# Kernel optimization log

Measured on AMD Instinct MI355X. Metric: run time of the kernel, lower is better.

Reference implementation:

```python
import jax, jax.numpy as jnp
import numpy as np

NUM_M = 512
NUM_T = 64
MAX_STEPS = 20
TAU = 1.0


def setup_inputs() -> dict:
    key = jax.random.key(0)
    ks = jax.random.split(key, 10)
    num_m, num_t = NUM_M, NUM_T
    inp = {
        "v_src": jax.random.normal(ks[0], (1, num_m), jnp.float32),
        "v_target": jax.random.normal(ks[1], (1, num_m), jnp.float32),
        # small-magnitude generators so matrix_exp stays well-conditioned
        "omegas": jax.random.normal(ks[2], (num_t, num_m, num_m), jnp.float32) * 0.01,
        "W1": jax.random.normal(ks[3], (2 * num_m, 256), jnp.float32) * (1.0 / np.sqrt(2 * num_m)),
        "b1": jnp.zeros((256,), jnp.float32),
        "W2": jax.random.normal(ks[4], (256, 128), jnp.float32) * (1.0 / np.sqrt(256)),
        "b2": jnp.zeros((128,), jnp.float32),
        "W3": jax.random.normal(ks[5], (128, num_t), jnp.float32) * (1.0 / np.sqrt(128)),
        "b3": jnp.zeros((num_t,), jnp.float32),
        # pre-sampled gumbel noise, one draw per step: [max_steps, B, num_t]
        "gumbel_noise": jax.random.gumbel(ks[6], (MAX_STEPS, 1, num_t), jnp.float32),
    }
    return inp


def reference(v_src, v_target, omegas, W1, b1, W2, b2, W3, b3, gumbel_noise):
    tgt_idx = jnp.argmax(v_target, axis=-1)  # [B]

    def mlp(x):
        h = jax.nn.relu(x @ W1 + b1)
        h = jax.nn.relu(h @ W2 + b2)
        return h @ W3 + b3  # [B, num_t]

    batched_expm = jax.vmap(jax.scipy.linalg.expm)

    def step(carry, g):
        v, done = carry  # v: [B, num_m], done: [B] bool
        x = jnp.concatenate([v, v_target], axis=-1)        # [B, 2*num_m]
        logits = mlp(x)                                     # [B, num_t]
        # gumbel_softmax(tau=1.0, hard=False)
        soft = jax.nn.softmax((logits + g) / TAU, axis=-1)
        omega_k = jnp.einsum('bt,tmk->bmk', soft, omegas)   # [B, m, m]
        R_k = batched_expm(omega_k)                         # [B, m, m]
        v_new = jnp.einsum('bmk,bk->bm', R_k, v)            # [B, m]
        # freeze state and zero-pad logits once the target marking was reached
        v_out = jnp.where(done[:, None], v, v_new)
        logits_out = jnp.where(done[:, None], jnp.zeros_like(logits), logits)
        done_new = done | (jnp.argmax(v_new, axis=-1) == tgt_idx)
        return (v_out, done_new), logits_out

    done0 = jnp.zeros((v_src.shape[0],), bool)
    (v_final, _), logits_seq = jax.lax.scan(step, (v_src, done0), gumbel_noise)
    # logits_seq: [max_steps, B, num_t]; B==1 -> [max_steps, num_t] (torch squeeze(0))
    return v_final, logits_seq[:, 0, :]
```

## Files before the change

kernel.cpp:

```cpp
#include <hip/hip_runtime.h>
#include <hip/hip_fp16.h>


#define NBLK 256
#define NTHR 512
#define NSTEP 20
#define NTAY 3
#define RBUF 4

typedef unsigned long long ull;

#define XW(buf, i) (X + ((((buf) << 8) + (i)) << 3))

__device__ __forceinline__ float wredsum(float p) {
#pragma unroll
  for (int off = 32; off > 0; off >>= 1) p += __shfl_xor(p, off, 64);
  return p;
}

__device__ __forceinline__ void wredsum2(float& p0, float& p1) {
#pragma unroll
  for (int off = 32; off > 0; off >>= 1) {
    float t0 = __shfl_xor(p0, off, 64);
    float t1 = __shfl_xor(p1, off, 64);
    p0 += t0;
    p1 += t1;
  }
}

__device__ __forceinline__ void publish2(ull* w, float v0, float v1, unsigned int tag2) {
  unsigned int u0 = (__float_as_uint(v0) & ~3u) | tag2;
  ull x = (ull)u0 | ((ull)__float_as_uint(v1) << 32);
  __hip_atomic_store(w, x, __ATOMIC_RELAXED, __HIP_MEMORY_SCOPE_AGENT);
}

__device__ __forceinline__ float2 poll2(ull* w, unsigned int tag2) {
  int it = 0;
  for (;;) {
    ull x = __hip_atomic_load(w, __ATOMIC_RELAXED, __HIP_MEMORY_SCOPE_AGENT);
    if ((unsigned int)(x & 3u) == tag2) {
      float2 r;
      r.x = __uint_as_float((unsigned int)x);
      r.y = __uint_as_float((unsigned int)(x >> 32));
      return r;
    }
    if (it == 0)      __builtin_amdgcn_s_sleep(1);
    else if (it == 1) __builtin_amdgcn_s_sleep(2);
    else              __builtin_amdgcn_s_sleep(4);
    if (it < 2) ++it;
  }
}

__device__ __forceinline__ void poll8(ull* w0, unsigned int tg, float* o) {
  ull x0 = 0, x1 = 0, x2 = 0, x3 = 0;
  bool g0 = false, g1 = false, g2 = false, g3 = false;
  int it = 0;
  for (;;) {
    if (!g0) { ull x = __hip_atomic_load(w0,      __ATOMIC_RELAXED, __HIP_MEMORY_SCOPE_AGENT); if ((unsigned int)(x & 3u) == tg) { x0 = x; g0 = true; } }
    if (!g1) { ull x = __hip_atomic_load(w0 + 8,  __ATOMIC_RELAXED, __HIP_MEMORY_SCOPE_AGENT); if ((unsigned int)(x & 3u) == tg) { x1 = x; g1 = true; } }
    if (!g2) { ull x = __hip_atomic_load(w0 + 16, __ATOMIC_RELAXED, __HIP_MEMORY_SCOPE_AGENT); if ((unsigned int)(x & 3u) == tg) { x2 = x; g2 = true; } }
    if (!g3) { ull x = __hip_atomic_load(w0 + 24, __ATOMIC_RELAXED, __HIP_MEMORY_SCOPE_AGENT); if ((unsigned int)(x & 3u) == tg) { x3 = x; g3 = true; } }
    if (g0 && g1 && g2 && g3) break;
    if (it == 0)      __builtin_amdgcn_s_sleep(1);
    else if (it == 1) __builtin_amdgcn_s_sleep(2);
    else              __builtin_amdgcn_s_sleep(4);
    if (it < 2) ++it;
  }
  o[0] = __uint_as_float((unsigned int)x0); o[1] = __uint_as_float((unsigned int)(x0 >> 32));
  o[2] = __uint_as_float((unsigned int)x1); o[3] = __uint_as_float((unsigned int)(x1 >> 32));
  o[4] = __uint_as_float((unsigned int)x2); o[5] = __uint_as_float((unsigned int)(x2 >> 32));
  o[6] = __uint_as_float((unsigned int)x3); o[7] = __uint_as_float((unsigned int)(x3 >> 32));
}

__global__ __launch_bounds__(NTHR) void petri_kernel(
    const float* __restrict__ vsrc, const float* __restrict__ vtgt,
    const float* __restrict__ omg,  const float* __restrict__ W1,
    const float* __restrict__ b1,   const float* __restrict__ W2,
    const float* __restrict__ b2,   const float* __restrict__ W3,
    const float* __restrict__ b3,   const float* __restrict__ gum,
    ull* __restrict__ X, float* __restrict__ out) {
  __shared__ __half2 oh[64 * 512];
  __shared__ __align__(16) float A0_s[512];
  __shared__ __align__(16) float A1_s[512];
  __shared__ __align__(16) float v_loc[512];
  __shared__ float tgt_s[512];
  __shared__ float w1c_s[1024];
  __shared__ float gum_s[NSTEP * 64];
  __shared__ float b2_s[128], b3_s[64];
  __shared__ float soft_s[64], h1_s[256], h2_s[128];
  __shared__ float redp[512];
  __shared__ float rf8[8];
  __shared__ int   ri8[8];
  __shared__ float cB_s[1];
  __shared__ int   bc[1];

  const int b = blockIdx.x, tid = threadIdx.x;
  const int wv = tid >> 6, ln = tid & 63;

  v_loc[tid] = vsrc[tid];
  tgt_s[tid] = vtgt[tid];
  w1c_s[tid] = W1[tid * 256 + b];
  w1c_s[tid + 512] = W1[(tid + 512) * 256 + b];
  for (int i = tid; i < NSTEP * 64; i += NTHR) gum_s[i] = gum[i];
  if (tid >= NTHR - 128) {
    int j = tid - (NTHR - 128);
    b2_s[j] = b2[j];
    if (j < 64) b3_s[j] = b3[j];
  }
  float w2r[64];
  {
    const int o = tid & 127, q = tid >> 7;
    const float* p = W2 + ((q << 6) * 128) + o;
#pragma unroll
    for (int i = 0; i < 64; ++i) w2r[i] = p[i * 128];
  }
  float w3r[16];
  {
    const int o = tid & 63, q = tid >> 6;
    const float* p = W3 + ((q << 4) * 64) + o;
#pragma unroll
    for (int i = 0; i < 16; ++i) w3r[i] = p[i * 64];
  }
  {
    const int tq = tid >> 7;
    const int c4 = (tid & 127) << 2;
    const float* rp = omg + (b << 10) + c4;
#pragma unroll 4
    for (int g = 0; g < 16; ++g) {
      const int t = (g << 2) + tq;
      const float* p = rp + t * 262144;
      const float4 f0 = *(const float4*)(p);
      const float4 f1 = *(const float4*)(p + 512);
      __half2* dst = oh + t * 512 + c4;
      dst[0] = __floats2half2_rn(f0.x, f1.x);
      dst[1] = __floats2half2_rn(f0.y, f1.y);
      dst[2] = __floats2half2_rn(f0.z, f1.z);
      dst[3] = __floats2half2_rn(f0.w, f1.w);
    }
  }
  __syncthreads();

  {
    float p = tgt_s[tid] * w1c_s[tid + 512];
    p = wredsum(p);
    if (ln == 0) rf8[wv] = p;
    __syncthreads();
    if (tid == 0) {
      float a = b1[b];
      for (int q = 0; q < 8; ++q) a += rf8[q];
      cB_s[0] = a;
    }
    __syncthreads();
  }

  int tgtIdx;
  {
    float v = tgt_s[tid]; int ix = tid;
#pragma unroll
    for (int off = 32; off > 0; off >>= 1) {
      float ov = __shfl_xor(v, off, 64); int oi = __shfl_xor(ix, off, 64);
      if (ov > v || (ov == v && oi < ix)) { v = ov; ix = oi; }
    }
    if (ln == 0) { rf8[wv] = v; ri8[wv] = ix; }
    __syncthreads();
    if (tid == 0) {
      float bv = rf8[0]; int bix = ri8[0];
      for (int q = 1; q < 8; ++q)
        if (rf8[q] > bv || (rf8[q] == bv && ri8[q] < bix)) { bv = rf8[q]; bix = ri8[q]; }
      bc[0] = bix;
    }
    __syncthreads();
    tgtIdx = bc[0];
    __syncthreads();
  }

  float vreg[8], w1t[8];
  if (wv == 0) {
    const int l8 = ln << 3;
#pragma unroll
    for (int k = 0; k < 8; ++k) { vreg[k] = v_loc[l8 + k]; w1t[k] = w1c_s[l8 + k]; }
  }

  int d = 0;
  int r = 0;

  for (int s = 0; s < NSTEP; ++s) {
    if (d) {
      if (b == 0 && tid < 64) out[512 + s * 64 + tid] = 0.0f;
      continue;
    }

    {
      const int buf = r & (RBUF - 1);
      const unsigned int tg = (unsigned int)((r >> 2) & 3);
      if (wv == 0) {
        float p = 0.f;
#pragma unroll
        for (int k = 0; k < 8; ++k) p = fmaf(vreg[k], w1t[k], p);
        p = wredsum(p);
        if (ln == 0) {
          float h = fmaxf(p + cB_s[0], 0.f);
          publish2(XW(buf, b), h, h, tg);
        }
      }
      if (tid < 256) h1_s[tid] = poll2(XW(buf, tid), tg).x;
      __syncthreads();
      ++r;
    }

    {
      const int q = tid >> 7;
      float a = 0.f;
      const float* hp = h1_s + (q << 6);
#pragma unroll
      for (int i = 0; i < 64; ++i) a = fmaf(hp[i], w2r[i], a);
      redp[tid] = a;
    }
    __syncthreads();
    if (tid < 128) {
      float rr = redp[tid] + redp[tid + 128] + redp[tid + 256] + redp[tid + 384] + b2_s[tid];
      h2_s[tid] = fmaxf(rr, 0.f);
    }
    __syncthreads();
    {
      const int q = tid >> 6;
      float a = 0.f;
      const float* hp = h2_s + (q << 4);
#pragma unroll
      for (int i = 0; i < 16; ++i) a = fmaf(hp[i], w3r[i], a);
      redp[tid] = a;
    }
    __syncthreads();
    if (tid < 64) {
      float a = b3_s[tid];
#pragma unroll
      for (int q = 0; q < 8; ++q) a += redp[tid + (q << 6)];
      float lg = a + gum_s[s * 64 + tid];
      float mx = lg;
#pragma unroll
      for (int off = 32; off > 0; off >>= 1) mx = fmaxf(mx, __shfl_xor(mx, off, 64));
      float e = __expf(lg - mx);
      float sm = e;
#pragma unroll
      for (int off = 32; off > 0; off >>= 1) sm += __shfl_xor(sm, off, 64);
      soft_s[tid] = e / sm;
      if (b == 0) out[512 + s * 64 + tid] = a;
    }
    __syncthreads();

    {
      float a0 = 0.f, a1 = 0.f;
#pragma unroll 8
      for (int t = 0; t < 64; ++t) {
        float2 xy = __half22float2(oh[t * 512 + tid]);
        float sv = soft_s[t];
        a0 = fmaf(sv, xy.x, a0);
        a1 = fmaf(sv, xy.y, a1);
      }
      A0_s[tid] = a0; A1_s[tid] = a1;
    }
    __syncthreads();

    if (wv == 0) {
      const int l8 = ln << 3;
      float wreg[8];
#pragma unroll
      for (int k = 0; k < 8; ++k) wreg[k] = vreg[k];
      float acc0 = 0.f, acc1 = 0.f;
#pragma unroll
      for (int n = 1; n <= NTAY; ++n) {
        const int rr = r + (n - 1);
        const int buf = rr & (RBUF - 1);
        const unsigned int tg = (unsigned int)((rr >> 2) & 3);
        const float4 a00 = *(const float4*)(A0_s + l8);
        const float4 a01 = *(const float4*)(A0_s + l8 + 4);
        const float4 a10 = *(const float4*)(A1_s + l8);
        const float4 a11 = *(const float4*)(A1_s + l8 + 4);
        float p0 = 0.f, p1 = 0.f;
        p0 = fmaf(a00.x, wreg[0], p0); p0 = fmaf(a00.y, wreg[1], p0);
        p0 = fmaf(a00.z, wreg[2], p0); p0 = fmaf(a00.w, wreg[3], p0);
        p0 = fmaf(a01.x, wreg[4], p0); p0 = fmaf(a01.y, wreg[5], p0);
        p0 = fmaf(a01.z, wreg[6], p0); p0 = fmaf(a01.w, wreg[7], p0);
        p1 = fmaf(a10.x, wreg[0], p1); p1 = fmaf(a10.y, wreg[1], p1);
        p1 = fmaf(a10.z, wreg[2], p1); p1 = fmaf(a10.w, wreg[3], p1);
        p1 = fmaf(a11.x, wreg[4], p1); p1 = fmaf(a11.y, wreg[5], p1);
        p1 = fmaf(a11.z, wreg[6], p1); p1 = fmaf(a11.w, wreg[7], p1);
        wredsum2(p0, p1);
        if (ln == 0) {
          float s0, s1;
          if (n == 1) {
            s0 = p0; s1 = p1;
            acc0 = v_loc[(b << 1)] + s0;
            acc1 = v_loc[(b << 1) + 1] + s1;
          } else {
            const float inv = (n == 2) ? 0.5f : (1.0f / 3.0f);
            s0 = p0 * inv; s1 = p1 * inv;
            acc0 += s0; acc1 += s1;
          }
          const float q0 = (n < NTAY) ? s0 : acc0;
          const float q1 = (n < NTAY) ? s1 : acc1;
          publish2(XW(buf, b), q0, q1, tg);
        }
        poll8(XW(buf, (ln << 2)), tg, wreg);
      }
#pragma unroll
      for (int k = 0; k < 8; ++k) vreg[k] = wreg[k];
      *(float4*)(v_loc + l8)     = make_float4(wreg[0], wreg[1], wreg[2], wreg[3]);
      *(float4*)(v_loc + l8 + 4) = make_float4(wreg[4], wreg[5], wreg[6], wreg[7]);
      float mv = wreg[0]; int mi = l8;
#pragma unroll
      for (int k = 1; k < 8; ++k) if (wreg[k] > mv) { mv = wreg[k]; mi = l8 + k; }
#pragma unroll
      for (int off = 32; off > 0; off >>= 1) {
        float ov = __shfl_xor(mv, off, 64); int oi = __shfl_xor(mi, off, 64);
        if (ov > mv || (ov == mv && oi < mi)) { mv = ov; mi = oi; }
      }
      if (ln == 0) bc[0] = (mi == tgtIdx) ? 1 : 0;
    }
    __syncthreads();
    if (bc[0]) d = 1;
    r += NTAY;
  }

  if (b == 0) out[tid] = v_loc[tid];
}

extern "C" void kernel_launch(void* const* d_in, const int* in_sizes, int n_in,
                              void* d_out, int out_size, void* d_ws, size_t ws_size,
                              hipStream_t stream) {
  (void)in_sizes; (void)n_in; (void)out_size; (void)ws_size;
  petri_kernel<<<dim3(NBLK), dim3(NTHR), 0, stream>>>(
      (const float*)d_in[0], (const float*)d_in[1], (const float*)d_in[2],
      (const float*)d_in[3], (const float*)d_in[4], (const float*)d_in[5],
      (const float*)d_in[6], (const float*)d_in[7], (const float*)d_in[8],
      (const float*)d_in[9], (ull*)d_ws, (float*)d_out);
}
```

Baseline: 343.0 us.

## Fuse next-step first MLP layer into expm exchange via fixed-point atomic accumulation

Each block now scatters its two new state entries, multiplied by its rows of W1, into global 64-bit accumulators using fixed-point atomicAdds that pack a count and a biased integer sum. Waves 1-4 poll these accumulators to build the next step's h1 while wave 0 finishes the Taylor exchange, which removes the separate per-step publish/poll round for layer 1. It also splits dot-product accumulators for ILP and swizzles the A0/A1 shared-memory layout so the float4 reads stay hoisted out of the Taylor loop. The fixed-point quantization of h1 changes numerics slightly and adds atomic contention across 256 blocks.

Result: slower. 962.1 us (+180.5%).

```diff
diff --git a/kernel.cpp b/kernel.cpp
--- a/kernel.cpp
+++ b/kernel.cpp
@@ -11,6 +11,11 @@
 typedef unsigned long long ull;
 
 #define XW(buf, i) (X + ((((buf) << 8) + (i)) << 3))
+#define AW(p, i)   (X + 8192 + ((((p) << 8) + (i)) << 3))
+
+#define SCALE_F   4194304.0f
+#define INV_SCALE 2.384185791015625e-07f
+#define M44 ((1ull << 44) - 1)
 
 __device__ __forceinline__ float wredsum(float p) {
 #pragma unroll
@@ -85,13 +90,15 @@
   __shared__ __align__(16) float v_loc[512];
   __shared__ float tgt_s[512];
   __shared__ float w1c_s[1024];
+  __shared__ float w1r0_s[256], w1r1_s[256];
+  __shared__ float cB_s[256];
   __shared__ float gum_s[NSTEP * 64];
   __shared__ float b2_s[128], b3_s[64];
   __shared__ float soft_s[64], h1_s[256], h2_s[128];
   __shared__ float redp[512];
-  __shared__ float rf8[8];
+  __shared__ float rf8[8], rf8b[8];
   __shared__ int   ri8[8];
-  __shared__ float cB_s[1];
+  __shared__ int   goflag;
   __shared__ int   bc[1];
 
   const int b = blockIdx.x, tid = threadIdx.x;
@@ -101,11 +108,18 @@
   tgt_s[tid] = vtgt[tid];
   w1c_s[tid] = W1[tid * 256 + b];
   w1c_s[tid + 512] = W1[(tid + 512) * 256 + b];
+  if (tid < 256) w1r0_s[tid] = W1[(b << 1) * 256 + tid];
+  else           w1r1_s[tid - 256] = W1[((b << 1) + 1) * 256 + (tid - 256)];
   for (int i = tid; i < NSTEP * 64; i += NTHR) gum_s[i] = gum[i];
   if (tid >= NTHR - 128) {
     int j = tid - (NTHR - 128);
     b2_s[j] = b2[j];
     if (j < 64) b3_s[j] = b3[j];
+  }
+  if (tid == 0) {
+    goflag = 0;
+    __hip_atomic_store(AW(0, b), 0ull, __ATOMIC_RELAXED, __HIP_MEMORY_SCOPE_AGENT);
+    __hip_atomic_store(AW(1, b), 0ull, __ATOMIC_RELAXED, __HIP_MEMORY_SCOPE_AGENT);
   }
   float w2r[64];
   {
@@ -141,14 +155,21 @@
   __syncthreads();
 
   {
-    float p = tgt_s[tid] * w1c_s[tid + 512];
-    p = wredsum(p);
-    if (ln == 0) rf8[wv] = p;
+    float p0 = tgt_s[tid] * w1c_s[tid + 512];
+    float p1 = v_loc[tid] * w1c_s[tid];
+    wredsum2(p0, p1);
+    if (ln == 0) { rf8[wv] = p0; rf8b[wv] = p1; }
     __syncthreads();
     if (tid == 0) {
-      float a = b1[b];
-      for (int q = 0; q < 8; ++q) a += rf8[q];
-      cB_s[0] = a;
+      float cB = b1[b], dv = 0.f;
+      for (int q = 0; q < 8; ++q) { cB += rf8[q]; dv += rf8b[q]; }
+      float h0 = fmaxf(dv + cB, 0.f);
+      publish2(XW(0, b), h0, cB, 0u);
+    }
+    if (tid < 256) {
+      float2 g = poll2(XW(0, tid), 0u);
+      h1_s[tid] = g.x;
+      cB_s[tid] = g.y;
     }
     __syncthreads();
   }
@@ -174,15 +195,17 @@
     __syncthreads();
   }
 
-  float vreg[8], w1t[8];
+  float vreg[8];
   if (wv == 0) {
     const int l8 = ln << 3;
 #pragma unroll
-    for (int k = 0; k < 8; ++k) { vreg[k] = v_loc[l8 + k]; w1t[k] = w1c_s[l8 + k]; }
-  }
+    for (int k = 0; k < 8; ++k) vreg[k] = v_loc[l8 + k];
+  }
+
+  ull prevA = 0, prevB = 0, expA = 0, expB = 0;
 
   int d = 0;
-  int r = 0;
+  int r = 1;
 
   for (int s = 0; s < NSTEP; ++s) {
     if (d) {
@@ -191,30 +214,17 @@
     }
 
     {
-      const int buf = r & (RBUF - 1);
-      const unsigned int tg = (unsigned int)((r >> 2) & 3);
-      if (wv == 0) {
-        float p = 0.f;
-#pragma unroll
-        for (int k = 0; k < 8; ++k) p = fmaf(vreg[k], w1t[k], p);
-        p = wredsum(p);
-        if (ln == 0) {
-          float h = fmaxf(p + cB_s[0], 0.f);
-          publish2(XW(buf, b), h, h, tg);
-        }
-      }
-      if (tid < 256) h1_s[tid] = poll2(XW(buf, tid), tg).x;
-      __syncthreads();
-      ++r;
-    }
-
-    {
       const int q = tid >> 7;
-      float a = 0.f;
       const float* hp = h1_s + (q << 6);
-#pragma unroll
-      for (int i = 0; i < 64; ++i) a = fmaf(hp[i], w2r[i], a);
-      redp[tid] = a;
+      float a0 = 0.f, a1 = 0.f, a2 = 0.f, a3 = 0.f;
+#pragma unroll
+      for (int i = 0; i < 64; i += 4) {
+        a0 = fmaf(hp[i],     w2r[i],     a0);
+        a1 = fmaf(hp[i + 1], w2r[i + 1], a1);
+        a2 = fmaf(hp[i + 2], w2r[i + 2], a2);
+        a3 = fmaf(hp[i + 3], w2r[i + 3], a3);
+      }
+      redp[tid] = (a0 + a1) + (a2 + a3);
     }
     __syncthreads();
     if (tid < 128) {
@@ -224,11 +234,14 @@
     __syncthreads();
     {
       const int q = tid >> 6;
-      float a = 0.f;
       const float* hp = h2_s + (q << 4);
-#pragma unroll
-      for (int i = 0; i < 16; ++i) a = fmaf(hp[i], w3r[i], a);
-      redp[tid] = a;
+      float a0 = 0.f, a1 = 0.f;
+#pragma unroll
+      for (int i = 0; i < 16; i += 2) {
+        a0 = fmaf(hp[i],     w3r[i],     a0);
+        a1 = fmaf(hp[i + 1], w3r[i + 1], a1);
+      }
+      redp[tid] = a0 + a1;
     }
     __syncthreads();
     if (tid < 64) {
@@ -249,20 +262,33 @@
     __syncthreads();
 
     {
-      float a0 = 0.f, a1 = 0.f;
+      float a0 = 0.f, a1 = 0.f, c0 = 0.f, c1 = 0.f;
 #pragma unroll 8
-      for (int t = 0; t < 64; ++t) {
-        float2 xy = __half22float2(oh[t * 512 + tid]);
-        float sv = soft_s[t];
-        a0 = fmaf(sv, xy.x, a0);
-        a1 = fmaf(sv, xy.y, a1);
-      }
-      A0_s[tid] = a0; A1_s[tid] = a1;
+      for (int t = 0; t < 64; t += 2) {
+        float2 xy0 = __half22float2(oh[t * 512 + tid]);
+        float2 xy1 = __half22float2(oh[(t + 1) * 512 + tid]);
+        float s0 = soft_s[t], s1 = soft_s[t + 1];
+        a0 = fmaf(s0, xy0.x, a0);
+        c0 = fmaf(s0, xy0.y, c0);
+        a1 = fmaf(s1, xy1.x, a1);
+        c1 = fmaf(s1, xy1.y, c1);
+      }
+      const int kk = tid >> 2;
+      const int sj = ((kk ^ ((kk >> 3) & 7)) << 2) | (tid & 3);
+      A0_s[sj] = a0 + a1;
+      A1_s[sj] = c0 + c1;
     }
     __syncthreads();
 
     if (wv == 0) {
-      const int l8 = ln << 3;
+      const int xh = (ln >> 2) & 7;
+      const int p0i = (ln << 1) ^ xh;
+      const int p1i = ((ln << 1) + 1) ^ xh;
+      const float4* A0p = (const float4*)A0_s;
+      const float4* A1p = (const float4*)A1_s;
+      const float4 a00 = A0p[p0i], a01 = A0p[p1i];
+      const float4 a10 = A1p[p0i], a11 = A1p[p1i];
+      const float vb0 = v_loc[b << 1], vb1 = v_loc[(b << 1) + 1];
       float wreg[8];
 #pragma unroll
       for (int k = 0; k < 8; ++k) wreg[k] = vreg[k];
@@ -272,10 +298,6 @@
         const int rr = r + (n - 1);
         const int buf = rr & (RBUF - 1);
         const unsigned int tg = (unsigned int)((rr >> 2) & 3);
-        const float4 a00 = *(const float4*)(A0_s + l8);
-        const float4 a01 = *(const float4*)(A0_s + l8 + 4);
-        const float4 a10 = *(const float4*)(A1_s + l8);
-        const float4 a11 = *(const float4*)(A1_s + l8 + 4);
         float p0 = 0.f, p1 = 0.f;
         p0 = fmaf(a00.x, wreg[0], p0); p0 = fmaf(a00.y, wreg[1], p0);
         p0 = fmaf(a00.z, wreg[2], p0); p0 = fmaf(a00.w, wreg[3], p0);
@@ -290,8 +312,7 @@
           float s0, s1;
           if (n == 1) {
             s0 = p0; s1 = p1;
-            acc0 = v_loc[(b << 1)] + s0;
-            acc1 = v_loc[(b << 1) + 1] + s1;
+            acc0 = vb0 + s0; acc1 = vb1 + s1;
           } else {
             const float inv = (n == 2) ? 0.5f : (1.0f / 3.0f);
             s0 = p0 * inv; s1 = p1 * inv;
@@ -301,8 +322,23 @@
           const float q1 = (n < NTAY) ? s1 : acc1;
           publish2(XW(buf, b), q0, q1, tg);
         }
+        if (n == NTAY && s < NSTEP - 1) {
+          const float ac0 = __shfl(acc0, 0, 64);
+          const float ac1 = __shfl(acc1, 0, 64);
+          const int p = (s + 1) & 1;
+#pragma unroll
+          for (int k = 0; k < 4; ++k) {
+            const int j = (ln << 2) + k;
+            const float part = fmaf(ac0, w1r0_s[j], ac1 * w1r1_s[j]);
+            const int iv = __float2int_rn(part * SCALE_F) + (1 << 30);
+            atomicAdd(AW(p, j), (1ull << 44) + (ull)(unsigned)iv);
+          }
+        }
         poll8(XW(buf, (ln << 2)), tg, wreg);
-      }
+        if (n == 2 && ln == 0)
+          __hip_atomic_store(&goflag, s + 1, __ATOMIC_RELAXED, __HIP_MEMORY_SCOPE_WORKGROUP);
+      }
+      const int l8 = ln << 3;
 #pragma unroll
       for (int k = 0; k < 8; ++k) vreg[k] = wreg[k];
       *(float4*)(v_loc + l8)     = make_float4(wreg[0], wreg[1], wreg[2], wreg[3]);
@@ -316,6 +352,31 @@
         if (ov > mv || (ov == mv && oi < mi)) { mv = ov; mi = oi; }
       }
       if (ln == 0) bc[0] = (mi == tgtIdx) ? 1 : 0;
+    } else if (wv <= 4) {
+      if (s < NSTEP - 1) {
+        while (__hip_atomic_load(&goflag, __ATOMIC_RELAXED, __HIP_MEMORY_SCOPE_WORKGROUP) != s + 1)
+          __builtin_amdgcn_s_sleep(2);
+        const int j = ((wv - 1) << 6) + ln;
+        const int p = (s + 1) & 1;
+        ull target;
+        if (p) { expB += 256; target = expB; } else { expA += 256; target = expA; }
+        ull* w = AW(p, j);
+        ull x;
+        int it = 0;
+        for (;;) {
+          x = __hip_atomic_load(w, __ATOMIC_RELAXED, __HIP_MEMORY_SCOPE_AGENT);
+          if ((x >> 44) == target) break;
+          if (it == 0)      __builtin_amdgcn_s_sleep(1);
+          else if (it == 1) __builtin_amdgcn_s_sleep(2);
+          else              __builtin_amdgcn_s_sleep(4);
+          if (it < 2) ++it;
+        }
+        const ull pv = p ? prevB : prevA;
+        const long long dl = (long long)((x & M44) - (pv & M44));
+        const float h = (float)(dl - (256ll << 30)) * INV_SCALE + cB_s[j];
+        h1_s[j] = fmaxf(h, 0.f);
+        if (p) prevB = x; else prevA = x;
+      }
     }
     __syncthreads();
     if (bc[0]) d = 1;
```

## Pack exchange slots densely, hoist next-step h1 publish, buffer logits in LDS

Applied to the files above, without the earlier changes.

Exchange slots in the global workspace are packed contiguously instead of spread 64 bytes apart, so the four polled words share cache lines. The first-layer partial for the next step is computed and published right after the Taylor exchange rather than at the start of the next iteration, which removes one serial phase from the critical path. Logits are kept in shared memory and written once at the end, and the inner dot products use split accumulators to shorten FMA dependency chains. Dense packing may add false sharing between blocks writing neighbouring slots.

Result: slower. 381.8 us (+11.3%).

```diff
diff --git a/kernel.cpp b/kernel.cpp
--- a/kernel.cpp
+++ b/kernel.cpp
@@ -10,7 +10,7 @@
 
 typedef unsigned long long ull;
 
-#define XW(buf, i) (X + ((((buf) << 8) + (i)) << 3))
+#define XW(buf, i) (X + ((buf) << 8) + (i))
 
 __device__ __forceinline__ float wredsum(float p) {
 #pragma unroll
@@ -56,10 +56,10 @@
   bool g0 = false, g1 = false, g2 = false, g3 = false;
   int it = 0;
   for (;;) {
-    if (!g0) { ull x = __hip_atomic_load(w0,      __ATOMIC_RELAXED, __HIP_MEMORY_SCOPE_AGENT); if ((unsigned int)(x & 3u) == tg) { x0 = x; g0 = true; } }
-    if (!g1) { ull x = __hip_atomic_load(w0 + 8,  __ATOMIC_RELAXED, __HIP_MEMORY_SCOPE_AGENT); if ((unsigned int)(x & 3u) == tg) { x1 = x; g1 = true; } }
-    if (!g2) { ull x = __hip_atomic_load(w0 + 16, __ATOMIC_RELAXED, __HIP_MEMORY_SCOPE_AGENT); if ((unsigned int)(x & 3u) == tg) { x2 = x; g2 = true; } }
-    if (!g3) { ull x = __hip_atomic_load(w0 + 24, __ATOMIC_RELAXED, __HIP_MEMORY_SCOPE_AGENT); if ((unsigned int)(x & 3u) == tg) { x3 = x; g3 = true; } }
+    if (!g0) { ull x = __hip_atomic_load(w0,     __ATOMIC_RELAXED, __HIP_MEMORY_SCOPE_AGENT); if ((unsigned int)(x & 3u) == tg) { x0 = x; g0 = true; } }
+    if (!g1) { ull x = __hip_atomic_load(w0 + 1, __ATOMIC_RELAXED, __HIP_MEMORY_SCOPE_AGENT); if ((unsigned int)(x & 3u) == tg) { x1 = x; g1 = true; } }
+    if (!g2) { ull x = __hip_atomic_load(w0 + 2, __ATOMIC_RELAXED, __HIP_MEMORY_SCOPE_AGENT); if ((unsigned int)(x & 3u) == tg) { x2 = x; g2 = true; } }
+    if (!g3) { ull x = __hip_atomic_load(w0 + 3, __ATOMIC_RELAXED, __HIP_MEMORY_SCOPE_AGENT); if ((unsigned int)(x & 3u) == tg) { x3 = x; g3 = true; } }
     if (g0 && g1 && g2 && g3) break;
     if (it == 0)      __builtin_amdgcn_s_sleep(1);
     else if (it == 1) __builtin_amdgcn_s_sleep(2);
@@ -89,6 +89,7 @@
   __shared__ float b2_s[128], b3_s[64];
   __shared__ float soft_s[64], h1_s[256], h2_s[128];
   __shared__ float redp[512];
+  __shared__ float llog[NSTEP * 64];
   __shared__ float rf8[8];
   __shared__ int   ri8[8];
   __shared__ float cB_s[1];
@@ -179,30 +180,27 @@
     const int l8 = ln << 3;
 #pragma unroll
     for (int k = 0; k < 8; ++k) { vreg[k] = v_loc[l8 + k]; w1t[k] = w1c_s[l8 + k]; }
+    float p = 0.f;
+#pragma unroll
+    for (int k = 0; k < 8; ++k) p = fmaf(vreg[k], w1t[k], p);
+    p = wredsum(p);
+    if (ln == 0) {
+      float h = fmaxf(p + cB_s[0], 0.f);
+      publish2(XW(0, b), h, h, 0u);
+    }
   }
 
   int d = 0;
+  int nAct = 0;
   int r = 0;
 
   for (int s = 0; s < NSTEP; ++s) {
-    if (d) {
-      if (b == 0 && tid < 64) out[512 + s * 64 + tid] = 0.0f;
-      continue;
-    }
+    if (d) continue;
+    nAct = s + 1;
 
     {
       const int buf = r & (RBUF - 1);
       const unsigned int tg = (unsigned int)((r >> 2) & 3);
-      if (wv == 0) {
-        float p = 0.f;
-#pragma unroll
-        for (int k = 0; k < 8; ++k) p = fmaf(vreg[k], w1t[k], p);
-        p = wredsum(p);
-        if (ln == 0) {
-          float h = fmaxf(p + cB_s[0], 0.f);
-          publish2(XW(buf, b), h, h, tg);
-        }
-      }
       if (tid < 256) h1_s[tid] = poll2(XW(buf, tid), tg).x;
       __syncthreads();
       ++r;
@@ -210,11 +208,16 @@
 
     {
       const int q = tid >> 7;
-      float a = 0.f;
       const float* hp = h1_s + (q << 6);
-#pragma unroll
-      for (int i = 0; i < 64; ++i) a = fmaf(hp[i], w2r[i], a);
-      redp[tid] = a;
+      float a0 = 0.f, a1 = 0.f, a2 = 0.f, a3 = 0.f;
+#pragma unroll
+      for (int i = 0; i < 64; i += 4) {
+        a0 = fmaf(hp[i],     w2r[i],     a0);
+        a1 = fmaf(hp[i + 1], w2r[i + 1], a1);
+        a2 = fmaf(hp[i + 2], w2r[i + 2], a2);
+        a3 = fmaf(hp[i + 3], w2r[i + 3], a3);
+      }
+      redp[tid] = (a0 + a1) + (a2 + a3);
     }
     __syncthreads();
     if (tid < 128) {
@@ -224,11 +227,14 @@
     __syncthreads();
     {
       const int q = tid >> 6;
-      float a = 0.f;
       const float* hp = h2_s + (q << 4);
-#pragma unroll
-      for (int i = 0; i < 16; ++i) a = fmaf(hp[i], w3r[i], a);
-      redp[tid] = a;
+      float a0 = 0.f, a1 = 0.f;
+#pragma unroll
+      for (int i = 0; i < 16; i += 2) {
+        a0 = fmaf(hp[i],     w3r[i],     a0);
+        a1 = fmaf(hp[i + 1], w3r[i + 1], a1);
+      }
+      redp[tid] = a0 + a1;
     }
     __syncthreads();
     if (tid < 64) {
@@ -244,25 +250,34 @@
 #pragma unroll
       for (int off = 32; off > 0; off >>= 1) sm += __shfl_xor(sm, off, 64);
       soft_s[tid] = e / sm;
-      if (b == 0) out[512 + s * 64 + tid] = a;
+      llog[s * 64 + tid] = a;
     }
     __syncthreads();
 
     {
-      float a0 = 0.f, a1 = 0.f;
+      float a0 = 0.f, a1 = 0.f, c0 = 0.f, c1 = 0.f;
 #pragma unroll 8
-      for (int t = 0; t < 64; ++t) {
-        float2 xy = __half22float2(oh[t * 512 + tid]);
-        float sv = soft_s[t];
-        a0 = fmaf(sv, xy.x, a0);
-        a1 = fmaf(sv, xy.y, a1);
-      }
-      A0_s[tid] = a0; A1_s[tid] = a1;
+      for (int t = 0; t < 64; t += 2) {
+        float2 xy0 = __half22float2(oh[t * 512 + tid]);
+        float2 xy1 = __half22float2(oh[(t + 1) * 512 + tid]);
+        float s0 = soft_s[t], s1 = soft_s[t + 1];
+        a0 = fmaf(s0, xy0.x, a0);
+        c0 = fmaf(s0, xy0.y, c0);
+        a1 = fmaf(s1, xy1.x, a1);
+        c1 = fmaf(s1, xy1.y, c1);
+      }
+      A0_s[tid] = a0 + a1;
+      A1_s[tid] = c0 + c1;
     }
     __syncthreads();
 
     if (wv == 0) {
       const int l8 = ln << 3;
+      const float4 a00 = *(const float4*)(A0_s + l8);
+      const float4 a01 = *(const float4*)(A0_s + l8 + 4);
+      const float4 a10 = *(const float4*)(A1_s + l8);
+      const float4 a11 = *(const float4*)(A1_s + l8 + 4);
+      const float vb0 = v_loc[b << 1], vb1 = v_loc[(b << 1) + 1];
       float wreg[8];
 #pragma unroll
       for (int k = 0; k < 8; ++k) wreg[k] = vreg[k];
@@ -272,10 +287,6 @@
         const int rr = r + (n - 1);
         const int buf = rr & (RBUF - 1);
         const unsigned int tg = (unsigned int)((rr >> 2) & 3);
-        const float4 a00 = *(const float4*)(A0_s + l8);
-        const float4 a01 = *(const float4*)(A0_s + l8 + 4);
-        const float4 a10 = *(const float4*)(A1_s + l8);
-        const float4 a11 = *(const float4*)(A1_s + l8 + 4);
         float p0 = 0.f, p1 = 0.f;
         p0 = fmaf(a00.x, wreg[0], p0); p0 = fmaf(a00.y, wreg[1], p0);
         p0 = fmaf(a00.z, wreg[2], p0); p0 = fmaf(a00.w, wreg[3], p0);
@@ -290,8 +301,7 @@
           float s0, s1;
           if (n == 1) {
             s0 = p0; s1 = p1;
-            acc0 = v_loc[(b << 1)] + s0;
-            acc1 = v_loc[(b << 1) + 1] + s1;
+            acc0 = vb0 + s0; acc1 = vb1 + s1;
           } else {
             const float inv = (n == 2) ? 0.5f : (1.0f / 3.0f);
             s0 = p0 * inv; s1 = p1 * inv;
@@ -303,6 +313,18 @@
         }
         poll8(XW(buf, (ln << 2)), tg, wreg);
       }
+      if (s + 1 < NSTEP) {
+        const int rh = r + NTAY;
+        const unsigned int tgh = (unsigned int)((rh >> 2) & 3);
+        float ph = 0.f;
+#pragma unroll
+        for (int k = 0; k < 8; ++k) ph = fmaf(wreg[k], w1t[k], ph);
+        ph = wredsum(ph);
+        if (ln == 0) {
+          float h = fmaxf(ph + cB_s[0], 0.f);
+          publish2(XW(rh & (RBUF - 1), b), h, h, tgh);
+        }
+      }
 #pragma unroll
       for (int k = 0; k < 8; ++k) vreg[k] = wreg[k];
       *(float4*)(v_loc + l8)     = make_float4(wreg[0], wreg[1], wreg[2], wreg[3]);
@@ -322,7 +344,11 @@
     r += NTAY;
   }
 
-  if (b == 0) out[tid] = v_loc[tid];
+  if (b == 0) {
+    out[tid] = v_loc[tid];
+    for (int i = tid; i < NSTEP * 64; i += NTHR)
+      out[512 + i] = (i < nAct * 64) ? llog[i] : 0.0f;
+  }
 }
 
 extern "C" void kernel_launch(void* const* d_in, const int* in_sizes, int n_in,
```
